# Optimization experiments

Measured on AMD Instinct MI355X. Metric: run time of the kernel, lower is better.

The kernel has to match this reference:

```python
import jax, jax.numpy as jnp
import numpy as np

H = 4          # num attention heads
LRELU = 0.2    # DGL GATConv leaky-relu slope
N_GT, N_AG = 100000, 20000
E_GT, E_COMM = 640000, 320000
D_GT, D_AG = 32, 64
VIS, COMM, MSG, OUT = 64, 128, 64, 5
NUM_COMM_STEPS = 2


def _leaky(x):
    return jnp.where(x >= 0, x, LRELU * x)


def gat(feat_src, feat_dst, w_src, w_dst, a_l, a_r, bias, src, dst, n_dst, dh):
    """Bipartite DGL GATConv: residual=Identity (in_dst == H*dh), activation=ReLU."""
    fs = (feat_src @ w_src).reshape(-1, H, dh)   # [Ns,H,dh]
    fd = (feat_dst @ w_dst).reshape(-1, H, dh)   # [Nd,H,dh]
    el = (fs * a_l[None]).sum(-1)                # [Ns,H]
    er = (fd * a_r[None]).sum(-1)                # [Nd,H]
    e = _leaky(el[src] + er[dst])                # [E,H]
    emax = jax.ops.segment_max(e, dst, num_segments=n_dst)
    ex = jnp.exp(e - emax[dst])
    denom = jax.ops.segment_sum(ex, dst, num_segments=n_dst)
    a = ex / denom[dst]                          # edge softmax over in-edges
    rst = jax.ops.segment_sum(fs[src] * a[..., None], dst, num_segments=n_dst)
    rst = rst + feat_dst.reshape(n_dst, H, dh)   # identity residual
    rst = rst + bias.reshape(1, H, dh)
    return jax.nn.relu(rst).reshape(n_dst, H * dh)


def gru(x, h, w_ih, w_hh, b_ih, b_hh):
    gi = x @ w_ih + b_ih
    gh = h @ w_hh + b_hh
    i_r, i_z, i_n = jnp.split(gi, 3, axis=1)
    h_r, h_z, h_n = jnp.split(gh, 3, axis=1)
    r = jax.nn.sigmoid(i_r + h_r)
    zg = jax.nn.sigmoid(i_z + h_z)
    n = jnp.tanh(i_n + r * h_n)
    return (1.0 - zg) * n + zg * h


def setup_inputs() -> dict:
    key = jax.random.key(0)
    ks = jax.random.split(key, 32)
    def w(k, shp):
        return (jax.random.normal(k, shp, dtype=jnp.float32) / np.sqrt(shp[0])).astype(jnp.float32)
    dh1, dh2 = VIS // H, COMM // H
    inp = {
        'feat_gt': jax.random.normal(ks[0], (N_GT, D_GT), dtype=jnp.float32),
        'feat_agent': jax.random.normal(ks[1], (N_AG, D_AG), dtype=jnp.float32),
        'z': jax.random.normal(ks[2], (N_AG, COMM), dtype=jnp.float32),
        'gt_src': jax.random.randint(ks[3], (E_GT,), 0, N_GT, dtype=jnp.int32),
        'gt_dst': jax.random.randint(ks[4], (E_GT,), 0, N_AG, dtype=jnp.int32),
        'comm_src': jax.random.randint(ks[5], (E_COMM,), 0, N_AG, dtype=jnp.int32),
        'comm_dst': jax.random.randint(ks[6], (E_COMM,), 0, N_AG, dtype=jnp.int32),
        # vis1 GATConv (gt->agent), out 64 = 4 heads x 16
        'w1_src': w(ks[7], (D_GT, VIS)), 'w1_dst': w(ks[8], (D_AG, VIS)),
        'a1_l': w(ks[9], (H, dh1)), 'a1_r': w(ks[10], (H, dh1)),
        'b1': jnp.zeros((VIS,), jnp.float32),
        'w2_src': w(ks[11], (D_GT, COMM)), 'w2_dst': w(ks[12], (VIS + D_AG, COMM)),
        'a2_l': w(ks[13], (H, dh2)), 'a2_r': w(ks[14], (H, dh2)),
        'b2': jnp.zeros((COMM,), jnp.float32),
        # comm f_enc: mlp([128,128,64]) with ReLU everywhere
        'enc_w1': w(ks[15], (COMM, 128)), 'enc_b1': jnp.zeros((128,), jnp.float32),
        'enc_w2': w(ks[16], (128, MSG)), 'enc_b2': jnp.zeros((MSG,), jnp.float32),
        # GRUCell(in=COMM+MSG=192, hidden=COMM=128), stored [in, 3*hidden]
        'gru_w_ih': w(ks[17], (COMM + MSG, 3 * COMM)),
        'gru_w_hh': w(ks[18], (COMM, 3 * COMM)),
        'gru_b_ih': jnp.zeros((3 * COMM,), jnp.float32),
        'gru_b_hh': jnp.zeros((3 * COMM,), jnp.float32),
        # f_out
        'out_w': w(ks[19], (COMM, OUT)), 'out_b': jnp.zeros((OUT,), jnp.float32),
    }
    return inp


def _forward(feat_gt, feat_agent, z, gt_src, gt_dst, comm_src, comm_dst,
             w1_src, w1_dst, a1_l, a1_r, b1,
             w2_src, w2_dst, a2_l, a2_r, b2,
             enc_w1, enc_b1, enc_w2, enc_b2,
             gru_w_ih, gru_w_hh, gru_b_ih, gru_b_hh,
             out_w, out_b):
    n_ag = feat_agent.shape[0]
    h_vis1 = gat(feat_gt, feat_agent, w1_src, w1_dst, a1_l, a1_r, b1,
                 gt_src, gt_dst, n_ag, VIS // H)
    dst2 = jnp.concatenate([h_vis1, feat_agent], axis=1)
    h = gat(feat_gt, dst2, w2_src, w2_dst, a2_l, a2_r, b2,
            gt_src, gt_dst, n_ag, COMM // H)
    deg = jax.ops.segment_sum(jnp.ones_like(comm_dst, dtype=jnp.float32),
                              comm_dst, num_segments=n_ag)
    denom = jnp.maximum(deg, 1.0)[:, None]
    zz = z
    for _ in range(NUM_COMM_STEPS):
        m = jax.nn.relu(jax.nn.relu(h @ enc_w1 + enc_b1) @ enc_w2 + enc_b2)  # per-node f_enc
        y = jax.ops.segment_sum(m[comm_src], comm_dst, num_segments=n_ag) / denom  # mailbox mean
        h = gru(jnp.concatenate([h, y], axis=1), zz, gru_w_ih, gru_w_hh, gru_b_ih, gru_b_hh)
        zz = h
    h_out = h @ out_w + out_b
    return h_out, zz


def reference(feat_gt, feat_agent, z, gt_src, gt_dst, comm_src, comm_dst,
              w1_src, w1_dst, a1_l, a1_r, b1,
              w2_src, w2_dst, a2_l, a2_r, b2,
              enc_w1, enc_b1, enc_w2, enc_b2,
              gru_w_ih, gru_w_hh, gru_b_ih, gru_b_hh,
              out_w, out_b):
    return _forward(feat_gt, feat_agent, z, gt_src, gt_dst, comm_src, comm_dst,
                    w1_src, w1_dst, a1_l, a1_r, b1,
                    w2_src, w2_dst, a2_l, a2_r, b2,
                    enc_w1, enc_b1, enc_w2, enc_b2,
                    gru_w_ih, gru_w_hh, gru_b_ih, gru_b_hh,
                    out_w, out_b)
```

## Files before the change

### kernel.cpp

```cpp
#include <hip/hip_runtime.h>
#include <math.h>

#define NHEAD 4
#define LRELU_S 0.2f
constexpr int N_GT = 100000, N_AG = 20000;
constexpr int E_GT = 640000, E_COMM = 320000;
constexpr int OUTD = 5;
constexpr int NBLK_SC = (N_AG + 255) / 256;
constexpr int MB_GT = (N_GT + 63) / 64;
constexpr int FS_TILES = 3 * MB_GT;
constexpr int ETILES  = (N_AG + 31) / 32;
constexpr int GGROUPS = (N_AG + 3) / 4;

constexpr long O_CNTP_GT = 0;
constexpr long O_CNTP_CM = 320000;
constexpr long O_FSB1    = 0;
constexpr long O_FSB2    = 3200000;
constexpr long O_EL1     = 12800000;
constexpr long O_EL2     = 13200000;
constexpr long O_ER1     = 14880000;
constexpr long O_RST2    = 17600000;
constexpr long O_DINV    = 20160000;
constexpr long O_OFFS_GT = 20180000;
constexpr long O_SRT_GT  = 20200004;
constexpr long O_OFFS_CM = 20840004;
constexpr long O_SRT_CM  = 20860008;
constexpr long O_PART    = 21180008;
constexpr long O_V       = 21220008;
constexpr long O_WB      = 21300000;
constexpr long O_RANK_GT = 21500000;
constexpr long O_RANK_CM = 22140000;
constexpr long O_M  = 10240000;
constexpr long O_Y  = 15360000;

constexpr long WB_FS  = 0;
constexpr long WB_E1  = 6144;
constexpr long WB_E2  = 22528;
constexpr long WB_RZ  = 30720;
constexpr long WB_GIN = 112640;
constexpr long WB_GHN = 137216;

using bf8      = __attribute__((ext_vector_type(8))) short;
using f32x4v   = __attribute__((ext_vector_type(4))) float;
using ushort8v = __attribute__((ext_vector_type(8))) unsigned short;

__device__ __forceinline__ unsigned short f2bf(float x) {
    unsigned u = __float_as_uint(x);
    u += 0x7FFFu + ((u >> 16) & 1u);
    return (unsigned short)(u >> 16);
}
__device__ __forceinline__ float bf2f(unsigned short u) {
    return __uint_as_float(((unsigned)u) << 16);
}

__global__ __launch_bounds__(256) void p0_k(
    const float* __restrict__ w1s, const float* __restrict__ w1d,
    const float* __restrict__ a1l, const float* __restrict__ a1r,
    const float* __restrict__ w2s, const float* __restrict__ w2d,
    const float* __restrict__ a2l, const float* __restrict__ a2r,
    const float* __restrict__ e1, const float* __restrict__ e2,
    const float* __restrict__ gih, const float* __restrict__ ghh,
    float* __restrict__ ws)
{
    const int tid = (int)(blockIdx.x * 256 + threadIdx.x);
    const int NT  = (int)(gridDim.x * 256);
    unsigned* wsu = reinterpret_cast<unsigned*>(ws);
    unsigned short* wb = reinterpret_cast<unsigned short*>(ws + O_WB);
    for (int i = tid; i < 640000; i += NT) wsu[O_CNTP_GT + i] = 0u;
    for (int i = tid; i < 153600; i += NT) {
        float val;
        if (i < 2048)        { long l = i;          long n = l / 32,  k = l % 32;  val = w1s[k * 64 + n]; }
        else if (i < 6144)   { long l = i - 2048;   long n = l / 32,  k = l % 32;  val = w2s[k * 128 + n]; }
        else if (i < 22528)  { long l = i - 6144;   long n = l / 128, k = l % 128; val = e1[k * 128 + n]; }
        else if (i < 30720)  { long l = i - 22528;  long n = l / 128, k = l % 128; val = e2[k * 64 + n]; }
        else if (i < 112640) { long l = i - 30720;  long n = l / 320, k = l % 320;
                               val = (k < 192) ? gih[k * 384 + n] : ghh[(k - 192) * 384 + n]; }
        else if (i < 137216) { long l = i - 112640; long n = l / 192, k = l % 192; val = gih[k * 384 + 256 + n]; }
        else                 { long l = i - 137216; long n = l / 128, k = l % 128; val = ghh[k * 384 + 256 + n]; }
        wb[i] = f2bf(val);
    }
    if (tid < 1024) {
        const int i = tid;
        const float *wp, *ap; int dh, local;
        if (i < 128)      { wp = w1s; ap = a1l; dh = 16; local = i; }
        else if (i < 384) { wp = w1d; ap = a1r; dh = 16; local = i - 128; }
        else if (i < 512) { wp = w2s; ap = a2l; dh = 32; local = i - 384; }
        else              { wp = w2d; ap = a2r; dh = 32; local = i - 512; }
        int k = local >> 2, hh = local & 3;
        float s = 0.f;
        for (int j = 0; j < dh; ++j) s += wp[k * (4 * dh) + hh * dh + j] * ap[hh * dh + j];
        ws[O_V + i] = s;
    }
}

__global__ __launch_bounds__(256) void p1_k(
    const int* __restrict__ gt_dst, const int* __restrict__ comm_dst,
    const float* __restrict__ feat_gt, const float* __restrict__ feat_agent,
    float* __restrict__ ws)
{
    const int tid = (int)(blockIdx.x * 256 + threadIdx.x);
    unsigned* wsu = reinterpret_cast<unsigned*>(ws);
    if (tid < E_GT) {
        wsu[O_RANK_GT + tid] = atomicAdd(wsu + O_CNTP_GT + (long)gt_dst[tid] * 16, 1u);
    } else if (tid < E_GT + E_COMM) {
        int j = tid - E_GT;
        wsu[O_RANK_CM + j] = atomicAdd(wsu + O_CNTP_CM + (long)comm_dst[j] * 16, 1u);
    }
    const float* v1  = ws + O_V;
    const float* v2  = ws + O_V + 384;
    const float* vr1 = ws + O_V + 128;
    float* el1 = ws + O_EL1;
    float* el2 = ws + O_EL2;
    float* er1 = ws + O_ER1;
    if (tid < N_GT) {
        const int i = tid;
        float a[8] = {};
        const float* fp = feat_gt + (long)i * 32;
        for (int k = 0; k < 32; ++k) {
            float x = fp[k];
#pragma unroll
            for (int j = 0; j < 4; ++j) a[j] += x * v1[4 * k + j];
#pragma unroll
            for (int j = 0; j < 4; ++j) a[4 + j] += x * v2[4 * k + j];
        }
        *reinterpret_cast<float4*>(el1 + 4l * i) = {a[0], a[1], a[2], a[3]};
        *reinterpret_cast<float4*>(el2 + 4l * i) = {a[4], a[5], a[6], a[7]};
    } else if (tid < N_GT + N_AG) {
        int r = tid - N_GT;
        float a0 = 0, a1 = 0, a2 = 0, a3 = 0;
        const float* fp = feat_agent + (long)r * 64;
        for (int k = 0; k < 64; ++k) {
            float x = fp[k];
            a0 += x * vr1[4 * k];     a1 += x * vr1[4 * k + 1];
            a2 += x * vr1[4 * k + 2]; a3 += x * vr1[4 * k + 3];
        }
        *reinterpret_cast<float4*>(er1 + 4l * r) = {a0, a1, a2, a3};
    }
}

__global__ __launch_bounds__(256) void p2_k(float* __restrict__ ws)
{
    __shared__ unsigned shu[256];
    unsigned* wsu = reinterpret_cast<unsigned*>(ws);
    const int b = (int)blockIdx.x, t = (int)threadIdx.x;
    const int g  = (b >= NBLK_SC) ? 1 : 0;
    const int cb = b - g * NBLK_SC;
    const int i  = cb * 256 + t;
    const unsigned* cnt = wsu + (g ? O_CNTP_CM : O_CNTP_GT);
    unsigned c = (i < N_AG) ? cnt[(long)i * 16] : 0u;
    if (g && i < N_AG) ws[O_DINV + i] = 1.0f / fmaxf((float)c, 1.0f);
    shu[t] = c;
    __syncthreads();
    for (int off = 1; off < 256; off <<= 1) {
        unsigned v = (t >= off) ? shu[t - off] : 0u;
        __syncthreads();
        shu[t] += v;
        __syncthreads();
    }
    unsigned* offs = wsu + (g ? O_OFFS_CM : O_OFFS_GT);
    if (i < N_AG) offs[i] = shu[t] - c;
    if (t == 255) wsu[O_PART + b] = shu[255];
}

__global__ __launch_bounds__(256) void p3_k(float* __restrict__ ws)
{
    __shared__ unsigned shu[128];
    unsigned* wsu = reinterpret_cast<unsigned*>(ws);
    const int b = (int)blockIdx.x, t = (int)threadIdx.x;
    const int g  = (b >= NBLK_SC) ? 1 : 0;
    const int cb = b - g * NBLK_SC;
    if (t < 128) shu[t] = (t < cb) ? wsu[O_PART + g * NBLK_SC + t] : 0u;
    __syncthreads();
    for (int off = 64; off >= 1; off >>= 1) {
        if (t < off) shu[t] += shu[t + off];
        __syncthreads();
    }
    const unsigned pre = shu[0];
    unsigned* offs = wsu + (g ? O_OFFS_CM : O_OFFS_GT);
    const int i = cb * 256 + t;
    if (i < N_AG) offs[i] += pre;
    if (b == NBLK_SC - 1 && t == 0)     wsu[O_OFFS_GT + N_AG] = E_GT;
    if (b == 2 * NBLK_SC - 1 && t == 0) wsu[O_OFFS_CM + N_AG] = E_COMM;
}

__global__ __launch_bounds__(256) void p4_k(
    const int* __restrict__ gt_src, const int* __restrict__ gt_dst,
    const int* __restrict__ comm_src, const int* __restrict__ comm_dst,
    const float* __restrict__ A, float* __restrict__ ws)
{
    unsigned* wsu = reinterpret_cast<unsigned*>(ws);
    const int t = (int)threadIdx.x;
    const int tid = (int)(blockIdx.x * 256 + t);
    if (tid < E_GT) {
        wsu[O_SRT_GT + wsu[O_OFFS_GT + gt_dst[tid]] + wsu[O_RANK_GT + tid]] = (unsigned)gt_src[tid];
    } else if (tid < E_GT + E_COMM) {
        int j = tid - E_GT;
        wsu[O_SRT_CM + wsu[O_OFFS_CM + comm_dst[j]] + wsu[O_RANK_CM + j]] = (unsigned)comm_src[j];
    }

    __shared__ __align__(16) unsigned short As[64][40];
    __shared__ __align__(16) unsigned short Bs[64][40];
    const unsigned short* Btc = reinterpret_cast<unsigned short*>(ws + O_WB) + WB_FS;
    unsigned short* fsb1 = reinterpret_cast<unsigned short*>(ws + O_FSB1);
    unsigned short* fsb2 = reinterpret_cast<unsigned short*>(ws + O_FSB2);
    const int lane = t & 63, wv = t >> 6;
    const int wm = wv & 1, wn = wv >> 1;
    const int quad = lane >> 4, l16 = lane & 15;
    const int rA = t >> 3, cA = (t & 7) * 4;
    const int rB = t >> 2, cB = (t & 3) * 8;
    const int tt = (int)blockIdx.x;
    if (tt >= FS_TILES) return;
    const int n0 = (tt % 3) * 64, m0 = (tt / 3) * 64;
#pragma unroll
    for (int half = 0; half < 2; ++half) {
        const int r = rA + half * 32;
        const int row = m0 + r;
        float4 v = {0.f, 0.f, 0.f, 0.f};
        if (row < N_GT) v = *reinterpret_cast<const float4*>(A + (long)row * 32 + cA);
        ushort4 bb;
        bb.x = f2bf(v.x); bb.y = f2bf(v.y); bb.z = f2bf(v.z); bb.w = f2bf(v.w);
        *reinterpret_cast<ushort4*>(&As[r][cA]) = bb;
    }
    *reinterpret_cast<ushort8v*>(&Bs[rB][cB]) =
        *reinterpret_cast<const ushort8v*>(Btc + (long)(n0 + rB) * 32 + cB);
    __syncthreads();
    f32x4v acc[2][2] = {};
    const bf8 a0 = *reinterpret_cast<const bf8*>(&As[wm * 32 + l16][quad * 8]);
    const bf8 a1 = *reinterpret_cast<const bf8*>(&As[wm * 32 + 16 + l16][quad * 8]);
    const bf8 b0v = *reinterpret_cast<const bf8*>(&Bs[wn * 32 + l16][quad * 8]);
    const bf8 b1v = *reinterpret_cast<const bf8*>(&Bs[wn * 32 + 16 + l16][quad * 8]);
    acc[0][0] = __builtin_amdgcn_mfma_f32_16x16x32_bf16(a0, b0v, acc[0][0], 0, 0, 0);
    acc[0][1] = __builtin_amdgcn_mfma_f32_16x16x32_bf16(a0, b1v, acc[0][1], 0, 0, 0);
    acc[1][0] = __builtin_amdgcn_mfma_f32_16x16x32_bf16(a1, b0v, acc[1][0], 0, 0, 0);
    acc[1][1] = __builtin_amdgcn_mfma_f32_16x16x32_bf16(a1, b1v, acc[1][1], 0, 0, 0);
#pragma unroll
    for (int mt = 0; mt < 2; ++mt)
#pragma unroll
        for (int nt = 0; nt < 2; ++nt)
#pragma unroll
            for (int r = 0; r < 4; ++r) {
                const int row = m0 + wm * 32 + mt * 16 + quad * 4 + r;
                const int col = n0 + wn * 32 + nt * 16 + l16;
                if (row < N_GT) {
                    unsigned short v16 = f2bf(acc[mt][nt][r]);
                    if (col < 64) fsb1[(long)row * 64 + col] = v16;
                    else          fsb2[(long)row * 128 + (col - 64)] = v16;
                }
            }
}

__global__ __launch_bounds__(256) void gat12_k(
    const unsigned* __restrict__ offs, const unsigned* __restrict__ ssrc,
    const float* __restrict__ el1, const float* __restrict__ er1,
    const float* __restrict__ el2,
    const unsigned short* __restrict__ fsb1, const unsigned short* __restrict__ fsb2,
    const float* __restrict__ feat_agent,
    const float* __restrict__ b1, const float* __restrict__ b2,
    const float* __restrict__ vr2, float* __restrict__ out)
{
    const int wid = threadIdx.x >> 6, lane = threadIdx.x & 63;
    const int d = blockIdx.x * 4 + wid;
    if (d >= N_AG) return;
    const int h = lane >> 4, ei = lane & 15;
    const unsigned beg = __builtin_amdgcn_readfirstlane(offs[d]);
    const unsigned end = __builtin_amdgcn_readfirstlane(offs[d + 1]);
    const unsigned smax = (unsigned)N_GT - 1u;

    float m = -INFINITY, s = 0.f, acc0 = 0.f;
    {
        const float er_h = er1[4l * d + h];
        for (unsigned base = beg; base < end; base += 16) {
            const unsigned na = min(16u, end - base);
            unsigned sv = ssrc[base + ((unsigned)ei < na ? (unsigned)ei : 0u)];
            sv = min(sv, smax);
            unsigned short fw[16];
#pragma unroll
            for (int j = 0; j < 16; ++j) {
                const unsigned sj = min(ssrc[min(base + (unsigned)j, end - 1u)], smax);
                fw[j] = fsb1[(long)sj * 64 + lane];
            }
            float xv = -INFINITY;
            if ((unsigned)ei < na) {
                float x = el1[4l * sv + h] + er_h;
                xv = (x >= 0.f) ? x : LRELU_S * x;
            }
            float cm = xv;
#pragma unroll
            for (int off = 1; off < 16; off <<= 1) cm = fmaxf(cm, __shfl_xor(cm, off));
            const float mn = fmaxf(m, cm);
            const float corr = __expf(m - mn);
            const float p = __expf(xv - mn);
            float ps = p;
#pragma unroll
            for (int off = 1; off < 16; off <<= 1) ps += __shfl_xor(ps, off);
            s = s * corr + ps;
            acc0 *= corr;
            m = mn;
#pragma unroll
            for (int j = 0; j < 16; ++j) {
                const float pj = __shfl(p, (h << 4) | j);
                acc0 += pj * bf2f(fw[j]);
            }
        }
    }
    const float inv1 = (s > 0.f) ? 1.f / s : 0.f;
    const float r1 = feat_agent[(long)d * 64 + lane];
    const float o = fmaxf(acc0 * inv1 + r1 + b1[lane], 0.f);

    float e0 = o * vr2[lane * 4 + 0] + r1 * vr2[(64 + lane) * 4 + 0];
    float e1v = o * vr2[lane * 4 + 1] + r1 * vr2[(64 + lane) * 4 + 1];
    float e2v = o * vr2[lane * 4 + 2] + r1 * vr2[(64 + lane) * 4 + 2];
    float e3v = o * vr2[lane * 4 + 3] + r1 * vr2[(64 + lane) * 4 + 3];
#pragma unroll
    for (int off = 1; off < 64; off <<= 1) {
        e0  += __shfl_xor(e0, off);
        e1v += __shfl_xor(e1v, off);
        e2v += __shfl_xor(e2v, off);
        e3v += __shfl_xor(e3v, off);
    }
    const float er_h2 = (h == 0) ? e0 : (h == 1) ? e1v : (h == 2) ? e2v : e3v;

    const int c0 = lane * 2;
    float m2 = -INFINITY, s2 = 0.f, A0 = 0.f, A1 = 0.f;
    for (unsigned base = beg; base < end; base += 16) {
        const unsigned na = min(16u, end - base);
        unsigned sv = ssrc[base + ((unsigned)ei < na ? (unsigned)ei : 0u)];
        sv = min(sv, smax);
        unsigned fw[16];
#pragma unroll
        for (int j = 0; j < 16; ++j) {
            const unsigned sj = min(ssrc[min(base + (unsigned)j, end - 1u)], smax);
            fw[j] = *reinterpret_cast<const unsigned*>(fsb2 + (long)sj * 128 + c0);
        }
        float xv = -INFINITY;
        if ((unsigned)ei < na) {
            float x = el2[4l * sv + h] + er_h2;
            xv = (x >= 0.f) ? x : LRELU_S * x;
        }
        float cm = xv;
#pragma unroll
        for (int off = 1; off < 16; off <<= 1) cm = fmaxf(cm, __shfl_xor(cm, off));
        const float mn = fmaxf(m2, cm);
        const float corr = __expf(m2 - mn);
        const float p = __expf(xv - mn);
        float ps = p;
#pragma unroll
        for (int off = 1; off < 16; off <<= 1) ps += __shfl_xor(ps, off);
        s2 = s2 * corr + ps;
        A0 *= corr; A1 *= corr;
        m2 = mn;
#pragma unroll
        for (int j = 0; j < 16; ++j) {
            const float pj = __shfl(p, (h << 4) | j);
            A0 += pj * __uint_as_float((fw[j] & 0xFFFFu) << 16);
            A1 += pj * __uint_as_float((fw[j] >> 16) << 16);
        }
    }
    const float inv2 = (s2 > 0.f) ? 1.f / s2 : 0.f;
    const float rox = __shfl(o, c0 & 63);
    const float roy = __shfl(o, (c0 + 1) & 63);
    float2 r;
    if (c0 < 64) { r.x = rox; r.y = roy; }
    else r = *reinterpret_cast<const float2*>(feat_agent + (long)d * 64 + (c0 - 64));
    float2 oo;
    oo.x = fmaxf(A0 * inv2 + r.x + b2[c0], 0.f);
    oo.y = fmaxf(A1 * inv2 + r.y + b2[c0 + 1], 0.f);
    *reinterpret_cast<float2*>(out + (long)d * 128 + c0) = oo;
}

__global__ __launch_bounds__(512) void enc_k(
    const float* __restrict__ h,
    const unsigned short* __restrict__ we1, const unsigned short* __restrict__ we2,
    const float* __restrict__ eb1, const float* __restrict__ eb2,
    unsigned short* __restrict__ mb)
{
    __shared__ __align__(16) unsigned short As[32][136];
    __shared__ __align__(16) unsigned short Ts[32][136];
    const int tid = (int)threadIdx.x;
    const int lane = tid & 63, w = tid >> 6;
    const int quad = lane >> 4, l16 = lane & 15;
    const int m0 = (int)blockIdx.x * 32;
#pragma unroll
    for (int it = 0; it < 2; ++it) {
        int idx = tid + it * 512;
        int row = idx >> 5, cc = (idx & 31) * 4;
        int grow = m0 + row;
        float4 v = {0.f, 0.f, 0.f, 0.f};
        if (grow < N_AG) v = *reinterpret_cast<const float4*>(h + (long)grow * 128 + cc);
        ushort4 b;
        b.x = f2bf(v.x); b.y = f2bf(v.y); b.z = f2bf(v.z); b.w = f2bf(v.w);
        *reinterpret_cast<ushort4*>(&As[row][cc]) = b;
    }
    __syncthreads();
    {
        const int j0 = w * 16;
        const unsigned short* p = we1 + (long)(j0 + l16) * 128 + quad * 8;
        bf8 bw[4];
#pragma unroll
        for (int i = 0; i < 4; ++i) bw[i] = *reinterpret_cast<const bf8*>(p + i * 32);
        f32x4v acc[2] = {};
#pragma unroll
        for (int i = 0; i < 4; ++i) {
            const int k0 = i * 32;
            const bf8 a0 = *reinterpret_cast<const bf8*>(&As[l16][k0 + quad * 8]);
            const bf8 a1 = *reinterpret_cast<const bf8*>(&As[16 + l16][k0 + quad * 8]);
            acc[0] = __builtin_amdgcn_mfma_f32_16x16x32_bf16(a0, bw[i], acc[0], 0, 0, 0);
            acc[1] = __builtin_amdgcn_mfma_f32_16x16x32_bf16(a1, bw[i], acc[1], 0, 0, 0);
        }
        const int j = j0 + l16;
        const float bj = eb1[j];
#pragma unroll
        for (int mt = 0; mt < 2; ++mt)
#pragma unroll
            for (int r = 0; r < 4; ++r)
                Ts[mt * 16 + quad * 4 + r][j] = f2bf(fmaxf(acc[mt][r] + bj, 0.f));
    }
    __syncthreads();
    if (w < 4) {
        const int j0 = w * 16;
        const unsigned short* p = we2 + (long)(j0 + l16) * 128 + quad * 8;
        bf8 bw[4];
#pragma unroll
        for (int i = 0; i < 4; ++i) bw[i] = *reinterpret_cast<const bf8*>(p + i * 32);
        f32x4v acc[2] = {};
#pragma unroll
        for (int i = 0; i < 4; ++i) {
            const int k0 = i * 32;
            const bf8 a0 = *reinterpret_cast<const bf8*>(&Ts[l16][k0 + quad * 8]);
            const bf8 a1 = *reinterpret_cast<const bf8*>(&Ts[16 + l16][k0 + quad * 8]);
            acc[0] = __builtin_amdgcn_mfma_f32_16x16x32_bf16(a0, bw[i], acc[0], 0, 0, 0);
            acc[1] = __builtin_amdgcn_mfma_f32_16x16x32_bf16(a1, bw[i], acc[1], 0, 0, 0);
        }
        const int j = j0 + l16;
        const float bj = eb2[j];
#pragma unroll
        for (int mt = 0; mt < 2; ++mt)
#pragma unroll
            for (int r = 0; r < 4; ++r) {
                const int row = m0 + mt * 16 + quad * 4 + r;
                if (row < N_AG)
                    mb[(long)row * 64 + j] = f2bf(fmaxf(acc[mt][r] + bj, 0.f));
            }
    }
}

__global__ __launch_bounds__(256) void gather_k(
    const unsigned* __restrict__ coffs, const unsigned* __restrict__ cssrc,
    const unsigned short* __restrict__ mb, const float* __restrict__ dinv,
    float* __restrict__ y)
{
    const int tid = (int)threadIdx.x;
    const int lane = tid & 63, w = tid >> 6;
    const int d = (int)blockIdx.x * 4 + w;
    if (d >= N_AG) return;
    const unsigned beg = coffs[d], endo = coffs[d + 1];
    const int ei = lane & 15;
    const unsigned smax = (unsigned)N_AG - 1u;
    float acc = 0.f;
    for (unsigned base = beg; base < endo; base += 32) {
        const unsigned rem = endo - base;
        const unsigned naA = min(16u, rem);
        const bool hasB = rem > 16u;
        unsigned svA = cssrc[base + ((unsigned)ei < naA ? (unsigned)ei : 0u)];
        svA = min(svA, smax);
        unsigned svB = 0u; unsigned naB = 0u;
        if (hasB) {
            naB = min(16u, rem - 16u);
            svB = cssrc[base + 16u + ((unsigned)ei < naB ? (unsigned)ei : 0u)];
            svB = min(svB, smax);
        }
        unsigned short fwA[16], fwB[16];
#pragma unroll
        for (int j = 0; j < 16; ++j) {
            const unsigned sj = (unsigned)__shfl((int)svA, j);
            fwA[j] = mb[(long)sj * 64 + lane];
        }
        if (hasB) {
#pragma unroll
            for (int j = 0; j < 16; ++j) {
                const unsigned sj = (unsigned)__shfl((int)svB, j);
                fwB[j] = mb[(long)sj * 64 + lane];
            }
        }
#pragma unroll
        for (int j = 0; j < 16; ++j)
            if ((unsigned)j < naA) acc += bf2f(fwA[j]);
        if (hasB) {
#pragma unroll
            for (int j = 0; j < 16; ++j)
                if ((unsigned)j < naB) acc += bf2f(fwB[j]);
        }
    }
    y[(long)d * 64 + lane] = acc * dinv[d];
}

__global__ __launch_bounds__(512) void gru_k(
    const float* __restrict__ h_in, const float* __restrict__ y, const float* zz,
    const unsigned short* __restrict__ wrz, const unsigned short* __restrict__ wgin,
    const unsigned short* __restrict__ wghn,
    const float* __restrict__ gbih, const float* __restrict__ gbhh,
    float* hout)
{
    __shared__ __align__(16) unsigned short As[32][328];
    const int tid = (int)threadIdx.x;
    const int lane = tid & 63, w = tid >> 6;
    const int quad = lane >> 4, l16 = lane & 15;
    const int m0 = (int)blockIdx.x * 32;
#pragma unroll
    for (int it = 0; it < 5; ++it) {
        int idx = tid + it * 512;
        int row = idx / 80, cc = (idx - row * 80) * 4;
        int grow = m0 + row;
        float4 v = {0.f, 0.f, 0.f, 0.f};
        if (grow < N_AG) {
            if (cc < 128)      v = *reinterpret_cast<const float4*>(h_in + (long)grow * 128 + cc);
            else if (cc < 192) v = *reinterpret_cast<const float4*>(y + (long)grow * 64 + (cc - 128));
            else               v = *reinterpret_cast<const float4*>(zz + (long)grow * 128 + (cc - 192));
        }
        ushort4 b;
        b.x = f2bf(v.x); b.y = f2bf(v.y); b.z = f2bf(v.z); b.w = f2bf(v.w);
        *reinterpret_cast<ushort4*>(&As[row][cc]) = b;
    }
    __syncthreads();

    f32x4v aR[2] = {}, aZ[2] = {}, aI[2] = {}, aH[2] = {};
    const int j0 = w * 16;
    const unsigned short* pR = wrz + (long)(j0 + l16) * 320 + quad * 8;
    const unsigned short* pZ = wrz + (long)(128 + j0 + l16) * 320 + quad * 8;
#pragma unroll
    for (int half = 0; half < 2; ++half) {
        bf8 bR[5], bZ[5];
#pragma unroll
        for (int i = 0; i < 5; ++i) {
            const int k0 = half * 160 + i * 32;
            bR[i] = *reinterpret_cast<const bf8*>(pR + k0);
            bZ[i] = *reinterpret_cast<const bf8*>(pZ + k0);
        }
#pragma unroll
        for (int i = 0; i < 5; ++i) {
            const int k0 = half * 160 + i * 32;
            const bf8 a0 = *reinterpret_cast<const bf8*>(&As[l16][k0 + quad * 8]);
            const bf8 a1 = *reinterpret_cast<const bf8*>(&As[16 + l16][k0 + quad * 8]);
            aR[0] = __builtin_amdgcn_mfma_f32_16x16x32_bf16(a0, bR[i], aR[0], 0, 0, 0);
            aR[1] = __builtin_amdgcn_mfma_f32_16x16x32_bf16(a1, bR[i], aR[1], 0, 0, 0);
            aZ[0] = __builtin_amdgcn_mfma_f32_16x16x32_bf16(a0, bZ[i], aZ[0], 0, 0, 0);
            aZ[1] = __builtin_amdgcn_mfma_f32_16x16x32_bf16(a1, bZ[i], aZ[1], 0, 0, 0);
        }
    }
    {
        const unsigned short* pI = wgin + (long)(j0 + l16) * 192 + quad * 8;
        bf8 bI[6];
#pragma unroll
        for (int i = 0; i < 6; ++i) bI[i] = *reinterpret_cast<const bf8*>(pI + i * 32);
#pragma unroll
        for (int i = 0; i < 6; ++i) {
            const int k0 = i * 32;
            const bf8 a0 = *reinterpret_cast<const bf8*>(&As[l16][k0 + quad * 8]);
            const bf8 a1 = *reinterpret_cast<const bf8*>(&As[16 + l16][k0 + quad * 8]);
            aI[0] = __builtin_amdgcn_mfma_f32_16x16x32_bf16(a0, bI[i], aI[0], 0, 0, 0);
            aI[1] = __builtin_amdgcn_mfma_f32_16x16x32_bf16(a1, bI[i], aI[1], 0, 0, 0);
        }
    }
    {
        const unsigned short* pH = wghn + (long)(j0 + l16) * 128 + quad * 8;
        bf8 bH[4];
#pragma unroll
        for (int i = 0; i < 4; ++i) bH[i] = *reinterpret_cast<const bf8*>(pH + i * 32);
#pragma unroll
        for (int i = 0; i < 4; ++i) {
            const int k0 = 192 + i * 32;
            const bf8 a0 = *reinterpret_cast<const bf8*>(&As[l16][k0 + quad * 8]);
            const bf8 a1 = *reinterpret_cast<const bf8*>(&As[16 + l16][k0 + quad * 8]);
            aH[0] = __builtin_amdgcn_mfma_f32_16x16x32_bf16(a0, bH[i], aH[0], 0, 0, 0);
            aH[1] = __builtin_amdgcn_mfma_f32_16x16x32_bf16(a1, bH[i], aH[1], 0, 0, 0);
        }
    }
    const int j = j0 + l16;
#pragma unroll
    for (int mt = 0; mt < 2; ++mt)
#pragma unroll
        for (int r = 0; r < 4; ++r) {
            const int row = m0 + mt * 16 + quad * 4 + r;
            if (row >= N_AG) continue;
            const float rr = 1.f / (1.f + __expf(-(aR[mt][r] + gbih[j] + gbhh[j])));
            const float zg = 1.f / (1.f + __expf(-(aZ[mt][r] + gbih[128 + j] + gbhh[128 + j])));
            const float nn = tanhf(aI[mt][r] + gbih[256 + j] + rr * (aH[mt][r] + gbhh[256 + j]));
            const float hp = zz[(long)row * 128 + j];
            hout[(long)row * 128 + j] = (1.f - zg) * nn + zg * hp;
        }
}

__global__ __launch_bounds__(256) void out_k(
    const float* __restrict__ h, const float* __restrict__ ow,
    const float* __restrict__ ob, float* __restrict__ out)
{
    const int gtid = (int)(blockIdx.x * 256 + threadIdx.x);
    float4* od = reinterpret_cast<float4*>(out + (long)N_AG * OUTD);
    const float4* hs = reinterpret_cast<const float4*>(h);
    if (gtid < N_AG * 32) od[gtid] = hs[gtid];
    if (gtid < N_AG) {
        float acc[OUTD];
#pragma unroll
        for (int j = 0; j < OUTD; ++j) acc[j] = ob[j];
        for (int k = 0; k < 128; ++k) {
            float v = h[(long)gtid * 128 + k];
#pragma unroll
            for (int j = 0; j < OUTD; ++j) acc[j] += v * ow[k * OUTD + j];
        }
#pragma unroll
        for (int j = 0; j < OUTD; ++j) out[(long)gtid * OUTD + j] = acc[j];
    }
}

extern "C" void kernel_launch(void* const* d_in, const int* in_sizes, int n_in,
                              void* d_out, int out_size, void* d_ws, size_t ws_size,
                              hipStream_t stream) {
    const float* feat_gt    = (const float*)d_in[0];
    const float* feat_agent = (const float*)d_in[1];
    const float* z_in       = (const float*)d_in[2];
    const int*   gt_src     = (const int*)d_in[3];
    const int*   gt_dst     = (const int*)d_in[4];
    const int*   comm_src   = (const int*)d_in[5];
    const int*   comm_dst   = (const int*)d_in[6];
    const float* w1_src = (const float*)d_in[7];
    const float* w1_dst = (const float*)d_in[8];
    const float* a1_l   = (const float*)d_in[9];
    const float* a1_r   = (const float*)d_in[10];
    const float* b1     = (const float*)d_in[11];
    const float* w2_src = (const float*)d_in[12];
    const float* w2_dst = (const float*)d_in[13];
    const float* a2_l   = (const float*)d_in[14];
    const float* a2_r   = (const float*)d_in[15];
    const float* b2     = (const float*)d_in[16];
    const float* enc_w1 = (const float*)d_in[17];
    const float* enc_b1 = (const float*)d_in[18];
    const float* enc_w2 = (const float*)d_in[19];
    const float* enc_b2 = (const float*)d_in[20];
    const float* gw_ih  = (const float*)d_in[21];
    const float* gw_hh  = (const float*)d_in[22];
    const float* gb_ih  = (const float*)d_in[23];
    const float* gb_hh  = (const float*)d_in[24];
    const float* out_w  = (const float*)d_in[25];
    const float* out_b  = (const float*)d_in[26];

    float* ws = (float*)d_ws;
    unsigned* wsu = (unsigned*)d_ws;
    unsigned short* wb = (unsigned short*)(ws + O_WB);
    float* out = (float*)d_out;

    float* hptr = ws + O_RST2;
    unsigned short* mb = (unsigned short*)(ws + O_M);
    float* yb = ws + O_Y;

    p0_k<<<dim3(2500), dim3(256), 0, stream>>>(w1_src, w1_dst, a1_l, a1_r,
                                               w2_src, w2_dst, a2_l, a2_r,
                                               enc_w1, enc_w2, gw_ih, gw_hh, ws);
    p1_k<<<dim3(3750), dim3(256), 0, stream>>>(gt_dst, comm_dst, feat_gt, feat_agent, ws);
    p2_k<<<dim3(2 * NBLK_SC), dim3(256), 0, stream>>>(ws);
    p3_k<<<dim3(2 * NBLK_SC), dim3(256), 0, stream>>>(ws);
    p4_k<<<dim3(FS_TILES), dim3(256), 0, stream>>>(gt_src, gt_dst, comm_src, comm_dst,
                                                   feat_gt, ws);

    gat12_k<<<dim3(GGROUPS), dim3(256), 0, stream>>>(
        wsu + O_OFFS_GT, wsu + O_SRT_GT,
        ws + O_EL1, ws + O_ER1, ws + O_EL2,
        (const unsigned short*)(ws + O_FSB1), (const unsigned short*)(ws + O_FSB2),
        feat_agent, b1, b2, ws + O_V + 512, hptr);

    for (int step = 0; step < 2; ++step) {
        const float* zz = (step == 0) ? z_in : hptr;
        enc_k<<<dim3(ETILES), dim3(512), 0, stream>>>(hptr, wb + WB_E1, wb + WB_E2,
                                                      enc_b1, enc_b2, mb);
        gather_k<<<dim3(GGROUPS), dim3(256), 0, stream>>>(wsu + O_OFFS_CM, wsu + O_SRT_CM,
                                                          mb, ws + O_DINV, yb);
        gru_k<<<dim3(ETILES), dim3(512), 0, stream>>>(hptr, yb, zz, wb + WB_RZ, wb + WB_GIN,
                                                      wb + WB_GHN, gb_ih, gb_hh, hptr);
    }
    out_k<<<dim3(2500), dim3(256), 0, stream>>>(hptr, out_w, out_b, out);
}
```

Measured before the change: 369.6 us.

## Per-lane edge softmax in GAT, widen gather batch, fuse output head into GRU

The GAT kernel now has every lane load all 16 edge logits itself and do the softmax max/sum serially, replacing the cross-lane shuffle reductions and per-edge broadcasts. The gather kernel handles 32 edges per iteration with scalar-uniform offsets and clamped indices instead of two shuffle-broadcast halves. The final linear head and the copy of the hidden state are fused into the last GRU launch through shared memory, which removes the separate out_k kernel. In exchange there are more redundant el loads per lane, more registers, and a serial 128-length dot product per output in the fused epilogue.

```diff
diff --git a/kernel.cpp b/kernel.cpp
--- a/kernel.cpp
+++ b/kernel.cpp
@@ -261,7 +261,7 @@
     const int wid = threadIdx.x >> 6, lane = threadIdx.x & 63;
     const int d = blockIdx.x * 4 + wid;
     if (d >= N_AG) return;
-    const int h = lane >> 4, ei = lane & 15;
+    const int h = lane >> 4;
     const unsigned beg = __builtin_amdgcn_readfirstlane(offs[d]);
     const unsigned end = __builtin_amdgcn_readfirstlane(offs[d + 1]);
     const unsigned smax = (unsigned)N_GT - 1u;
@@ -271,36 +271,32 @@
         const float er_h = er1[4l * d + h];
         for (unsigned base = beg; base < end; base += 16) {
             const unsigned na = min(16u, end - base);
-            unsigned sv = ssrc[base + ((unsigned)ei < na ? (unsigned)ei : 0u)];
-            sv = min(sv, smax);
-            unsigned short fw[16];
+            unsigned fw[16];
+            float x[16];
 #pragma unroll
             for (int j = 0; j < 16; ++j) {
                 const unsigned sj = min(ssrc[min(base + (unsigned)j, end - 1u)], smax);
                 fw[j] = fsb1[(long)sj * 64 + lane];
+                x[j]  = el1[4l * sj + h];
             }
-            float xv = -INFINITY;
-            if ((unsigned)ei < na) {
-                float x = el1[4l * sv + h] + er_h;
-                xv = (x >= 0.f) ? x : LRELU_S * x;
+            float cm = -INFINITY;
+#pragma unroll
+            for (int j = 0; j < 16; ++j) {
+                float xx = x[j] + er_h;
+                xx = (xx >= 0.f) ? xx : LRELU_S * xx;
+                x[j] = ((unsigned)j < na) ? xx : -INFINITY;
+                cm = fmaxf(cm, x[j]);
             }
-            float cm = xv;
-#pragma unroll
-            for (int off = 1; off < 16; off <<= 1) cm = fmaxf(cm, __shfl_xor(cm, off));
             const float mn = fmaxf(m, cm);
             const float corr = __expf(m - mn);
-            const float p = __expf(xv - mn);
-            float ps = p;
-#pragma unroll
-            for (int off = 1; off < 16; off <<= 1) ps += __shfl_xor(ps, off);
+            float ps = 0.f;
+#pragma unroll
+            for (int j = 0; j < 16; ++j) { const float p = __expf(x[j] - mn); x[j] = p; ps += p; }
             s = s * corr + ps;
             acc0 *= corr;
             m = mn;
 #pragma unroll
-            for (int j = 0; j < 16; ++j) {
-                const float pj = __shfl(p, (h << 4) | j);
-                acc0 += pj * bf2f(fw[j]);
-            }
+            for (int j = 0; j < 16; ++j) acc0 += x[j] * bf2f((unsigned short)fw[j]);
         }
     }
     const float inv1 = (s > 0.f) ? 1.f / s : 0.f;
@@ -324,36 +320,34 @@
     float m2 = -INFINITY, s2 = 0.f, A0 = 0.f, A1 = 0.f;
     for (unsigned base = beg; base < end; base += 16) {
         const unsigned na = min(16u, end - base);
-        unsigned sv = ssrc[base + ((unsigned)ei < na ? (unsigned)ei : 0u)];
-        sv = min(sv, smax);
         unsigned fw[16];
+        float x[16];
 #pragma unroll
         for (int j = 0; j < 16; ++j) {
             const unsigned sj = min(ssrc[min(base + (unsigned)j, end - 1u)], smax);
             fw[j] = *reinterpret_cast<const unsigned*>(fsb2 + (long)sj * 128 + c0);
-        }
-        float xv = -INFINITY;
-        if ((unsigned)ei < na) {
-            float x = el2[4l * sv + h] + er_h2;
-            xv = (x >= 0.f) ? x : LRELU_S * x;
-        }
-        float cm = xv;
-#pragma unroll
-        for (int off = 1; off < 16; off <<= 1) cm = fmaxf(cm, __shfl_xor(cm, off));
+            x[j]  = el2[4l * sj + h];
+        }
+        float cm = -INFINITY;
+#pragma unroll
+        for (int j = 0; j < 16; ++j) {
+            float xx = x[j] + er_h2;
+            xx = (xx >= 0.f) ? xx : LRELU_S * xx;
+            x[j] = ((unsigned)j < na) ? xx : -INFINITY;
+            cm = fmaxf(cm, x[j]);
+        }
         const float mn = fmaxf(m2, cm);
         const float corr = __expf(m2 - mn);
-        const float p = __expf(xv - mn);
-        float ps = p;
-#pragma unroll
-        for (int off = 1; off < 16; off <<= 1) ps += __shfl_xor(ps, off);
+        float ps = 0.f;
+#pragma unroll
+        for (int j = 0; j < 16; ++j) { const float p = __expf(x[j] - mn); x[j] = p; ps += p; }
         s2 = s2 * corr + ps;
         A0 *= corr; A1 *= corr;
         m2 = mn;
 #pragma unroll
         for (int j = 0; j < 16; ++j) {
-            const float pj = __shfl(p, (h << 4) | j);
-            A0 += pj * __uint_as_float((fw[j] & 0xFFFFu) << 16);
-            A1 += pj * __uint_as_float((fw[j] >> 16) << 16);
+            A0 += x[j] * __uint_as_float((fw[j] & 0xFFFFu) << 16);
+            A1 += x[j] * __uint_as_float((fw[j] >> 16) << 16);
         }
     }
     const float inv2 = (s2 > 0.f) ? 1.f / s2 : 0.f;
@@ -453,43 +447,21 @@
     const int lane = tid & 63, w = tid >> 6;
     const int d = (int)blockIdx.x * 4 + w;
     if (d >= N_AG) return;
-    const unsigned beg = coffs[d], endo = coffs[d + 1];
-    const int ei = lane & 15;
+    const unsigned beg  = __builtin_amdgcn_readfirstlane(coffs[d]);
+    const unsigned endo = __builtin_amdgcn_readfirstlane(coffs[d + 1]);
     const unsigned smax = (unsigned)N_AG - 1u;
     float acc = 0.f;
     for (unsigned base = beg; base < endo; base += 32) {
-        const unsigned rem = endo - base;
-        const unsigned naA = min(16u, rem);
-        const bool hasB = rem > 16u;
-        unsigned svA = cssrc[base + ((unsigned)ei < naA ? (unsigned)ei : 0u)];
-        svA = min(svA, smax);
-        unsigned svB = 0u; unsigned naB = 0u;
-        if (hasB) {
-            naB = min(16u, rem - 16u);
-            svB = cssrc[base + 16u + ((unsigned)ei < naB ? (unsigned)ei : 0u)];
-            svB = min(svB, smax);
-        }
-        unsigned short fwA[16], fwB[16];
-#pragma unroll
-        for (int j = 0; j < 16; ++j) {
-            const unsigned sj = (unsigned)__shfl((int)svA, j);
-            fwA[j] = mb[(long)sj * 64 + lane];
-        }
-        if (hasB) {
-#pragma unroll
-            for (int j = 0; j < 16; ++j) {
-                const unsigned sj = (unsigned)__shfl((int)svB, j);
-                fwB[j] = mb[(long)sj * 64 + lane];
-            }
-        }
-#pragma unroll
-        for (int j = 0; j < 16; ++j)
-            if ((unsigned)j < naA) acc += bf2f(fwA[j]);
-        if (hasB) {
-#pragma unroll
-            for (int j = 0; j < 16; ++j)
-                if ((unsigned)j < naB) acc += bf2f(fwB[j]);
-        }
+        const unsigned na = min(32u, endo - base);
+        unsigned short fw[32];
+#pragma unroll
+        for (int j = 0; j < 32; ++j) {
+            const unsigned sj = min(cssrc[min(base + (unsigned)j, endo - 1u)], smax);
+            fw[j] = mb[(long)sj * 64 + lane];
+        }
+#pragma unroll
+        for (int j = 0; j < 32; ++j)
+            if ((unsigned)j < na) acc += bf2f(fw[j]);
     }
     y[(long)d * 64 + lane] = acc * dinv[d];
 }
@@ -499,7 +471,8 @@
     const unsigned short* __restrict__ wrz, const unsigned short* __restrict__ wgin,
     const unsigned short* __restrict__ wghn,
     const float* __restrict__ gbih, const float* __restrict__ gbhh,
-    float* hout)
+    float* hout,
+    const float* __restrict__ ow, const float* __restrict__ ob, float* __restrict__ outp)
 {
     __shared__ __align__(16) unsigned short As[32][328];
     const int tid = (int)threadIdx.x;
@@ -576,39 +549,52 @@
         }
     }
     const int j = j0 + l16;
+    float hv[2][4];
 #pragma unroll
     for (int mt = 0; mt < 2; ++mt)
 #pragma unroll
         for (int r = 0; r < 4; ++r) {
             const int row = m0 + mt * 16 + quad * 4 + r;
-            if (row >= N_AG) continue;
-            const float rr = 1.f / (1.f + __expf(-(aR[mt][r] + gbih[j] + gbhh[j])));
-            const float zg = 1.f / (1.f + __expf(-(aZ[mt][r] + gbih[128 + j] + gbhh[128 + j])));
-            const float nn = tanhf(aI[mt][r] + gbih[256 + j] + rr * (aH[mt][r] + gbhh[256 + j]));
-            const float hp = zz[(long)row * 128 + j];
-            hout[(long)row * 128 + j] = (1.f - zg) * nn + zg * hp;
-        }
-}
-
-__global__ __launch_bounds__(256) void out_k(
-    const float* __restrict__ h, const float* __restrict__ ow,
-    const float* __restrict__ ob, float* __restrict__ out)
-{
-    const int gtid = (int)(blockIdx.x * 256 + threadIdx.x);
-    float4* od = reinterpret_cast<float4*>(out + (long)N_AG * OUTD);
-    const float4* hs = reinterpret_cast<const float4*>(h);
-    if (gtid < N_AG * 32) od[gtid] = hs[gtid];
-    if (gtid < N_AG) {
-        float acc[OUTD];
-#pragma unroll
-        for (int j = 0; j < OUTD; ++j) acc[j] = ob[j];
-        for (int k = 0; k < 128; ++k) {
-            float v = h[(long)gtid * 128 + k];
-#pragma unroll
-            for (int j = 0; j < OUTD; ++j) acc[j] += v * ow[k * OUTD + j];
-        }
-#pragma unroll
-        for (int j = 0; j < OUTD; ++j) out[(long)gtid * OUTD + j] = acc[j];
+            float v = 0.f;
+            if (row < N_AG) {
+                const float rr = 1.f / (1.f + __expf(-(aR[mt][r] + gbih[j] + gbhh[j])));
+                const float zg = 1.f / (1.f + __expf(-(aZ[mt][r] + gbih[128 + j] + gbhh[128 + j])));
+                const float nn = tanhf(aI[mt][r] + gbih[256 + j] + rr * (aH[mt][r] + gbhh[256 + j]));
+                const float hp = zz[(long)row * 128 + j];
+                v = (1.f - zg) * nn + zg * hp;
+            }
+            hv[mt][r] = v;
+        }
+
+    if (outp == nullptr) {
+#pragma unroll
+        for (int mt = 0; mt < 2; ++mt)
+#pragma unroll
+            for (int r = 0; r < 4; ++r) {
+                const int row = m0 + mt * 16 + quad * 4 + r;
+                if (row < N_AG) hout[(long)row * 128 + j] = hv[mt][r];
+            }
+    } else {
+        __syncthreads();
+        float* Hs = reinterpret_cast<float*>(&As[0][0]);
+#pragma unroll
+        for (int mt = 0; mt < 2; ++mt)
+#pragma unroll
+            for (int r = 0; r < 4; ++r)
+                Hs[(mt * 16 + quad * 4 + r) * 128 + j] = hv[mt][r];
+        __syncthreads();
+        for (int it = tid; it < 32 * 32; it += 512) {
+            const int row = it >> 5, c4 = (it & 31) * 4;
+            const float4 v = *reinterpret_cast<const float4*>(&Hs[row * 128 + c4]);
+            *reinterpret_cast<float4*>(outp + (long)N_AG * OUTD + (long)(m0 + row) * 128 + c4) = v;
+        }
+        for (int it = tid; it < 32 * OUTD; it += 512) {
+            const int row = it / OUTD, jj = it - row * OUTD;
+            float a = ob[jj];
+            const float* hr = &Hs[row * 128];
+            for (int k = 0; k < 128; ++k) a += hr[k] * ow[k * OUTD + jj];
+            outp[(long)(m0 + row) * OUTD + jj] = a;
+        }
     }
 }
 
@@ -674,7 +660,9 @@
         gather_k<<<dim3(GGROUPS), dim3(256), 0, stream>>>(wsu + O_OFFS_CM, wsu + O_SRT_CM,
                                                           mb, ws + O_DINV, yb);
         gru_k<<<dim3(ETILES), dim3(512), 0, stream>>>(hptr, yb, zz, wb + WB_RZ, wb + WB_GIN,
-                                                      wb + WB_GHN, gb_ih, gb_hh, hptr);
-    }
-    out_k<<<dim3(2500), dim3(256), 0, stream>>>(hptr, out_w, out_b, out);
-}
+                                                      wb + WB_GHN, gb_ih, gb_hh, hptr,
+                                                      (step == 1) ? out_w : nullptr,
+                                                      (step == 1) ? out_b : nullptr,
+                                                      (step == 1) ? out : nullptr);
+    }
+}
```

Result: no change. 370.2 us (+0.2%).
